# Performance work log

Measured on AMD Instinct MI355X. Metric: run time of the kernel, lower is better.

Reference implementation:

```python
import jax, jax.numpy as jnp
import numpy as np

DIM = 256
NUM_HEADS = 4
FRAMES = 8
B_ = 32768
INNER = DIM // 2              # 128
HEAD_DIM = INNER // NUM_HEADS # 32 (actual per-head dim in forward)
SCALE = (DIM // NUM_HEADS) ** -0.5  # faithful: init uses dim//num_heads = 64


def _rel_pos_index():
    # window_size = [FRAMES, 1, 1] -> index depends only on temporal offset
    d = np.arange(FRAMES)
    idx = d[:, None] - d[None, :] + (FRAMES - 1)  # [N, N] in [0, 2F-2]
    return jnp.asarray(idx, dtype=jnp.int32)


def setup_inputs() -> dict:
    key = jax.random.key(0)
    ks = jax.random.split(key, 5)
    x = jax.random.normal(ks[0], (B_, FRAMES, DIM), dtype=jnp.float32)
    qkv_w = jax.random.normal(ks[1], (DIM, INNER * 3), dtype=jnp.float32) * 0.02
    proj_w = jax.random.normal(ks[2], (INNER, DIM), dtype=jnp.float32) * 0.02
    proj_b = jnp.zeros((DIM,), dtype=jnp.float32)
    bias_table = jax.random.normal(ks[3], (2 * FRAMES - 1, NUM_HEADS), dtype=jnp.float32) * 0.02
    rel_index = _rel_pos_index()
    return {"x": x, "qkv_w": qkv_w, "proj_w": proj_w, "proj_b": proj_b,
            "bias_table": bias_table, "rel_index": rel_index}


def reference(x, qkv_w, proj_w, proj_b, bias_table, rel_index):
    B, N, C = x.shape
    h, hd = NUM_HEADS, HEAD_DIM
    qkv = (x @ qkv_w).reshape(B, N, 3, h, hd)
    qkv = jnp.transpose(qkv, (2, 0, 3, 1, 4))  # [3, B, h, N, hd]
    q, k, v = qkv[0], qkv[1], qkv[2]
    attn = jnp.einsum('bhnd,bhmd->bhnm', q * SCALE, k)  # [B, h, N, N]
    # gather relative position bias: [N, N, h] -> [h, N, N]
    bias = bias_table[rel_index[:N, :N]]  # [N, N, h]
    attn = attn + jnp.transpose(bias, (2, 0, 1))[None]
    attn = jax.nn.softmax(attn, axis=-1)
    out = jnp.einsum('bhnm,bhmd->bhnd', attn, v)       # [B, h, N, hd]
    out = jnp.transpose(out, (0, 2, 1, 3)).reshape(B, N, h * hd)  # [B, N, 128]
    return out @ proj_w + proj_b
```

## Files before the change

kernel.cpp:

```cpp
#include <hip/hip_runtime.h>
#include <hip/hip_bf16.h>

typedef short bf16x8 __attribute__((ext_vector_type(8)));
typedef float f32x4 __attribute__((ext_vector_type(4)));

#define B_TOT 32768
#define ROWS  128
#define NTHR  512

#define WSQ_ELT  0
#define WSP_ELT  98304

#define QK_STR   104
#define CH_STR   68
#define WQ_OFF   0
#define QK_OFF   24576
#define BIAS_OFF 59392
#define PB_OFF   60672
#define LDS_BYTES 61696

static __device__ __forceinline__ unsigned short f2b(float f) {
    __hip_bfloat16 h = __float2bfloat16(f);
    return reinterpret_cast<unsigned short&>(h);
}
static __device__ __forceinline__ float b2f(unsigned short u) {
    union { unsigned u; float f; } v; v.u = ((unsigned)u) << 16; return v.f;
}
static __device__ __forceinline__ void gload_lds16(const unsigned short* g, unsigned short* l) {
    __builtin_amdgcn_global_load_lds(
        (const __attribute__((address_space(1))) unsigned int*)g,
        (__attribute__((address_space(3))) unsigned int*)l, 16, 0, 0);
}

__global__ __launch_bounds__(256)
void prep_w(const float* __restrict__ qkv_w, const float* __restrict__ proj_w,
            unsigned short* __restrict__ ws)
{
    __shared__ float tile[64][65];
    const int bid = blockIdx.x;
    const float* src; unsigned short* dst; int ldw, ldk, tr0, tc0;
    if (bid < 24) {
        int kr = bid / 6, cg = bid % 6;
        src = qkv_w; dst = ws + WSQ_ELT; ldw = 384; ldk = 256;
        tr0 = kr * 64; tc0 = cg * 64;
    } else {
        int b = bid - 24; int kr = b / 4, cg = b % 4;
        src = proj_w; dst = ws + WSP_ELT; ldw = 256; ldk = 128;
        tr0 = kr * 64; tc0 = cg * 64;
    }
    const int t = threadIdx.x;
    #pragma unroll
    for (int i = 0; i < 16; ++i) {
        int idx = i * 256 + t;
        int r = idx >> 6, c = idx & 63;
        tile[r][c] = src[(size_t)(tr0 + r) * ldw + tc0 + c];
    }
    __syncthreads();
    #pragma unroll
    for (int i = 0; i < 2; ++i) {
        int idx = i * 256 + t;
        int c = idx >> 3, r0 = (idx & 7) * 8;
        union { unsigned short u[8]; uint4 v; } pk;
        #pragma unroll
        for (int j = 0; j < 8; ++j) pk.u[j] = f2b(tile[r0 + j][c]);
        *(uint4*)&dst[(size_t)(tc0 + c) * ldk + tr0 + r0] = pk.v;
    }
}

__global__ __launch_bounds__(NTHR, 4)
void ta_fused(const float* __restrict__ x,
              const unsigned short* __restrict__ ws,
              const float* __restrict__ proj_b,
              const float* __restrict__ bias_table,
              const int* __restrict__ rel_index,
              float* __restrict__ out)
{
    __shared__ __align__(16) char smem[LDS_BYTES];
    unsigned short* wqs = (unsigned short*)(smem + WQ_OFF);
    unsigned short* qks = (unsigned short*)(smem + QK_OFF);
    float* chunk  = (float*)(smem + QK_OFF);
    float* bias_s = (float*)(smem + BIAS_OFF);
    float* pbs    = (float*)(smem + PB_OFF);

    const unsigned short* wsq = ws + WSQ_ELT;
    const unsigned short* wsp = ws + WSP_ELT;

    const int tid = threadIdx.x;
    const int l   = tid & 63;
    const int w   = tid >> 6;
    const int l15 = l & 15;
    const int l4  = l >> 4;
    const long wg = blockIdx.x;

    bf16x8 af[8];
    {
        const float* xr = x + wg * (size_t)(ROWS * 256) + (size_t)(16 * w + l15) * 256;
        #pragma unroll
        for (int s = 0; s < 8; ++s) {
            f32x4 d0 = *(const f32x4*)(xr + s * 32 + l4 * 8);
            f32x4 d1 = *(const f32x4*)(xr + s * 32 + l4 * 8 + 4);
            union { unsigned short u[8]; bf16x8 v; } pk;
            #pragma unroll
            for (int j = 0; j < 4; ++j) pk.u[j] = f2b(d0[j]);
            #pragma unroll
            for (int j = 0; j < 4; ++j) pk.u[4 + j] = f2b(d1[j]);
            af[s] = pk.v;
        }
    }
    if (tid < 256) {
        int n = tid >> 5, m = (tid >> 2) & 7, hh = tid & 3;
        int ri = rel_index[n * 8 + m];
        bias_s[n * 40 + m * 5 + hh] = bias_table[ri * 4 + hh];
        pbs[tid] = proj_b[tid];
    }

    bf16x8 of0, of1, of2, of3;
    const f32x4 zero4 = {0.f, 0.f, 0.f, 0.f};

    #pragma unroll 1
    for (int h = 0; h < 4; ++h) {
        f32x4 acc[6];
        #pragma unroll
        for (int i = 0; i < 6; ++i) acc[i] = zero4;

        #pragma unroll
        for (int c = 0; c < 2; ++c) {
            __syncthreads();
            #pragma unroll
            for (int u = 0; u < 3; ++u) {
                int idx = u * NTHR + tid;
                int rr = idx >> 4, seg = idx & 15;
                int p = rr >> 5, wi = rr & 31;
                gload_lds16(&wsq[(size_t)(p * 128 + h * 32 + wi) * 256 + c * 128
                                 + ((seg ^ (rr & 7)) << 3)],
                            &wqs[rr * 128 + seg * 8]);
            }
            __syncthreads();
            #pragma unroll
            for (int ks2 = 0; ks2 < 4; ++ks2) {
                bf16x8 a = af[c * 4 + ks2];
                #pragma unroll
                for (int ct = 0; ct < 6; ++ct) {
                    int brow = ct * 16 + l15;
                    bf16x8 b = *(bf16x8*)&wqs[brow * 128 + (((ks2 * 4 + l4) ^ (brow & 7)) << 3)];
                    acc[ct] = __builtin_amdgcn_mfma_f32_16x16x32_bf16(a, b, acc[ct], 0, 0, 0);
                }
            }
        }
        #pragma unroll
        for (int ct = 0; ct < 6; ++ct)
          #pragma unroll
          for (int j = 0; j < 4; ++j) {
              int row = 16 * w + l4 * 4 + j;
              qks[row * QK_STR + ct * 16 + l15] = f2b(acc[ct][j]);
          }

        {
            const int r  = 16 * w + l15;
            const int rb = r & ~7;
            const int n  = r & 7;
            float qf[8];
            {
                bf16x8 qv = *(bf16x8*)&qks[r * QK_STR + l4 * 8];
                #pragma unroll
                for (int j = 0; j < 8; ++j) qf[j] = b2f((unsigned short)qv[j]);
            }
            float sp[8];
            #pragma unroll
            for (int m = 0; m < 8; ++m) {
                bf16x8 kv = *(bf16x8*)&qks[(rb + m) * QK_STR + 32 + l4 * 8];
                float s = 0.f;
                #pragma unroll
                for (int j = 0; j < 8; ++j) s += qf[j] * b2f((unsigned short)kv[j]);
                sp[m] = s;
            }
            #pragma unroll
            for (int m = 0; m < 8; ++m) {
                sp[m] += __shfl_xor(sp[m], 16);
                sp[m] += __shfl_xor(sp[m], 32);
            }
            float mx = -1e30f;
            #pragma unroll
            for (int m = 0; m < 8; ++m) {
                sp[m] = sp[m] * 0.125f + bias_s[n * 40 + m * 5 + h];
                mx = fmaxf(mx, sp[m]);
            }
            float sum = 0.f;
            #pragma unroll
            for (int m = 0; m < 8; ++m) { sp[m] = __expf(sp[m] - mx); sum += sp[m]; }
            float inv = 1.f / sum;
            float o[8] = {0.f,0.f,0.f,0.f,0.f,0.f,0.f,0.f};
            #pragma unroll
            for (int m = 0; m < 8; ++m) {
                bf16x8 vv = *(bf16x8*)&qks[(rb + m) * QK_STR + 64 + l4 * 8];
                #pragma unroll
                for (int j = 0; j < 8; ++j) o[j] += sp[m] * b2f((unsigned short)vv[j]);
            }
            bf16x8 ofr;
            #pragma unroll
            for (int j = 0; j < 8; ++j) ofr[j] = (short)f2b(o[j] * inv);
            if      (h == 0) of0 = ofr;
            else if (h == 1) of1 = ofr;
            else if (h == 2) of2 = ofr;
            else             of3 = ofr;
        }
    }

    __syncthreads();

    #pragma unroll 1
    for (int cc = 0; cc < 4; ++cc) {
        #pragma unroll
        for (int u = 0; u < 2; ++u) {
            int idx = u * NTHR + tid;
            int rr = idx >> 4, seg = idx & 15;
            gload_lds16(&wsp[(size_t)(cc * 64 + rr) * 128 + ((seg ^ (rr & 7)) << 3)],
                        &wqs[rr * 128 + seg * 8]);
        }
        __syncthreads();

        f32x4 acc2[4];
        #pragma unroll
        for (int i = 0; i < 4; ++i) acc2[i] = zero4;
        #pragma unroll
        for (int ctl = 0; ctl < 4; ++ctl) {
            int brow = ctl * 16 + l15;
            #pragma unroll
            for (int ks = 0; ks < 4; ++ks) {
                bf16x8 b = *(bf16x8*)&wqs[brow * 128 + (((ks * 4 + l4) ^ (brow & 7)) << 3)];
                bf16x8 a = (ks == 0) ? of0 : (ks == 1) ? of1 : (ks == 2) ? of2 : of3;
                acc2[ctl] = __builtin_amdgcn_mfma_f32_16x16x32_bf16(a, b, acc2[ctl], 0, 0, 0);
            }
        }
        #pragma unroll
        for (int ctl = 0; ctl < 4; ++ctl)
          #pragma unroll
          for (int j = 0; j < 4; ++j) {
              int row = 16 * w + l4 * 4 + j;
              int col = ctl * 16 + l15;
              chunk[row * CH_STR + col] = acc2[ctl][j] + pbs[cc * 64 + col];
          }
        __syncthreads();
        {
            float* og = out + wg * (size_t)(ROWS * 256) + cc * 64;
            #pragma unroll
            for (int i = 0; i < 4; ++i) {
                int f0 = i * NTHR + tid;
                int row = f0 >> 4, c4 = f0 & 15;
                f32x4 v = *(f32x4*)&chunk[row * CH_STR + c4 * 4];
                *(f32x4*)(og + (size_t)row * 256 + c4 * 4) = v;
            }
        }
    }
}

extern "C" void kernel_launch(void* const* d_in, const int* in_sizes, int n_in,
                              void* d_out, int out_size, void* d_ws, size_t ws_size,
                              hipStream_t stream)
{
    (void)in_sizes; (void)n_in; (void)ws_size; (void)out_size;
    const float* x  = (const float*)d_in[0];
    const float* qw = (const float*)d_in[1];
    const float* pw = (const float*)d_in[2];
    const float* pb = (const float*)d_in[3];
    const float* bt = (const float*)d_in[4];
    const int*   ri = (const int*)d_in[5];
    float* o = (float*)d_out;
    unsigned short* ws = (unsigned short*)d_ws;

    hipLaunchKernelGGL(prep_w, dim3(32), dim3(256), 0, stream, qw, pw, ws);
    hipLaunchKernelGGL(ta_fused, dim3(B_TOT / 16), dim3(NTHR), 0, stream,
                       x, ws, pb, bt, ri, o);
}
```

Baseline: 234.3 us.

## Double-buffer weight tiles in LDS to overlap global loads with MFMA

Splits the QKV and projection weight staging into half-width K chunks held in two LDS buffers. The next chunk is prefetched with global_load_lds while MFMAs consume the current one, and the prefetch chains across heads and into the projection phase. This aims to hide weight-load latency behind compute instead of stalling after each load. In exchange it adds more, smaller load phases and more complex barrier ordering.

```diff
diff --git a/kernel.cpp b/kernel.cpp
--- a/kernel.cpp
+++ b/kernel.cpp
@@ -11,10 +11,11 @@
 #define WSQ_ELT  0
 #define WSP_ELT  98304
 
+#define WQ0_OFF  0
+#define WQ1_OFF  12288
+#define QK_OFF   24576
 #define QK_STR   104
 #define CH_STR   68
-#define WQ_OFF   0
-#define QK_OFF   24576
 #define BIAS_OFF 59392
 #define PB_OFF   60672
 #define LDS_BYTES 61696
@@ -76,7 +77,8 @@
               float* __restrict__ out)
 {
     __shared__ __align__(16) char smem[LDS_BYTES];
-    unsigned short* wqs = (unsigned short*)(smem + WQ_OFF);
+    unsigned short* wq0 = (unsigned short*)(smem + WQ0_OFF);
+    unsigned short* wq1 = (unsigned short*)(smem + WQ1_OFF);
     unsigned short* qks = (unsigned short*)(smem + QK_OFF);
     float* chunk  = (float*)(smem + QK_OFF);
     float* bias_s = (float*)(smem + BIAS_OFF);
@@ -92,6 +94,32 @@
     const int l4  = l >> 4;
     const long wg = blockIdx.x;
 
+    auto stage1 = [&](int h, int c2, unsigned short* buf) {
+        {
+            int rr = tid >> 3, seg = tid & 7;
+            int p = rr >> 5, wi = rr & 31;
+            gload_lds16(&wsq[(size_t)(p * 128 + h * 32 + wi) * 256 + c2 * 64
+                             + ((seg ^ (rr & 7)) << 3)],
+                        &buf[rr * 64 + seg * 8]);
+        }
+        if (tid < 256) {
+            int idx = NTHR + tid;
+            int rr = idx >> 3, seg = idx & 7;
+            int p = rr >> 5, wi = rr & 31;
+            gload_lds16(&wsq[(size_t)(p * 128 + h * 32 + wi) * 256 + c2 * 64
+                             + ((seg ^ (rr & 7)) << 3)],
+                        &buf[rr * 64 + seg * 8]);
+        }
+    };
+    auto stage2 = [&](int cc, int kh, unsigned short* buf) {
+        int rr = tid >> 3, seg = tid & 7;
+        gload_lds16(&wsp[(size_t)(cc * 64 + rr) * 128 + kh * 64
+                         + ((seg ^ (rr & 7)) << 3)],
+                    &buf[rr * 64 + seg * 8]);
+    };
+
+    stage1(0, 0, wq0);
+
     bf16x8 af[8];
     {
         const float* xr = x + wg * (size_t)(ROWS * 256) + (size_t)(16 * w + l15) * 256;
@@ -124,25 +152,20 @@
         for (int i = 0; i < 6; ++i) acc[i] = zero4;
 
         #pragma unroll
-        for (int c = 0; c < 2; ++c) {
+        for (int c2 = 0; c2 < 4; ++c2) {
+            unsigned short* cur = (c2 & 1) ? wq1 : wq0;
+            unsigned short* nxt = (c2 & 1) ? wq0 : wq1;
             __syncthreads();
-            #pragma unroll
-            for (int u = 0; u < 3; ++u) {
-                int idx = u * NTHR + tid;
-                int rr = idx >> 4, seg = idx & 15;
-                int p = rr >> 5, wi = rr & 31;
-                gload_lds16(&wsq[(size_t)(p * 128 + h * 32 + wi) * 256 + c * 128
-                                 + ((seg ^ (rr & 7)) << 3)],
-                            &wqs[rr * 128 + seg * 8]);
-            }
-            __syncthreads();
-            #pragma unroll
-            for (int ks2 = 0; ks2 < 4; ++ks2) {
-                bf16x8 a = af[c * 4 + ks2];
+            if (c2 < 3)      stage1(h, c2 + 1, nxt);
+            else if (h < 3)  stage1(h + 1, 0, nxt);
+            else             stage2(0, 0, nxt);
+            #pragma unroll
+            for (int ks2 = 0; ks2 < 2; ++ks2) {
+                bf16x8 a = af[c2 * 2 + ks2];
                 #pragma unroll
                 for (int ct = 0; ct < 6; ++ct) {
                     int brow = ct * 16 + l15;
-                    bf16x8 b = *(bf16x8*)&wqs[brow * 128 + (((ks2 * 4 + l4) ^ (brow & 7)) << 3)];
+                    bf16x8 b = *(bf16x8*)&cur[brow * 64 + (((ks2 * 4 + l4) ^ (brow & 7)) << 3)];
                     acc[ct] = __builtin_amdgcn_mfma_f32_16x16x32_bf16(a, b, acc[ct], 0, 0, 0);
                 }
             }
@@ -206,29 +229,33 @@
         }
     }
 
-    __syncthreads();
-
     #pragma unroll 1
     for (int cc = 0; cc < 4; ++cc) {
-        #pragma unroll
-        for (int u = 0; u < 2; ++u) {
-            int idx = u * NTHR + tid;
-            int rr = idx >> 4, seg = idx & 15;
-            gload_lds16(&wsp[(size_t)(cc * 64 + rr) * 128 + ((seg ^ (rr & 7)) << 3)],
-                        &wqs[rr * 128 + seg * 8]);
-        }
         __syncthreads();
+        stage2(cc, 1, wq1);
 
         f32x4 acc2[4];
         #pragma unroll
         for (int i = 0; i < 4; ++i) acc2[i] = zero4;
         #pragma unroll
-        for (int ctl = 0; ctl < 4; ++ctl) {
-            int brow = ctl * 16 + l15;
-            #pragma unroll
-            for (int ks = 0; ks < 4; ++ks) {
-                bf16x8 b = *(bf16x8*)&wqs[brow * 128 + (((ks * 4 + l4) ^ (brow & 7)) << 3)];
-                bf16x8 a = (ks == 0) ? of0 : (ks == 1) ? of1 : (ks == 2) ? of2 : of3;
+        for (int ks = 0; ks < 2; ++ks) {
+            bf16x8 a = (ks == 0) ? of0 : of1;
+            #pragma unroll
+            for (int ctl = 0; ctl < 4; ++ctl) {
+                int brow = ctl * 16 + l15;
+                bf16x8 b = *(bf16x8*)&wq0[brow * 64 + (((ks * 4 + l4) ^ (brow & 7)) << 3)];
+                acc2[ctl] = __builtin_amdgcn_mfma_f32_16x16x32_bf16(a, b, acc2[ctl], 0, 0, 0);
+            }
+        }
+        __syncthreads();
+        if (cc < 3) stage2(cc + 1, 0, wq0);
+        #pragma unroll
+        for (int ks = 0; ks < 2; ++ks) {
+            bf16x8 a = (ks == 0) ? of2 : of3;
+            #pragma unroll
+            for (int ctl = 0; ctl < 4; ++ctl) {
+                int brow = ctl * 16 + l15;
+                bf16x8 b = *(bf16x8*)&wq1[brow * 64 + (((ks * 4 + l4) ^ (brow & 7)) << 3)];
                 acc2[ctl] = __builtin_amdgcn_mfma_f32_16x16x32_bf16(a, b, acc2[ctl], 0, 0, 0);
             }
         }
```

After: 214.6 us. -8.4%, faster.

## Double-buffer QKV and projection weight tiles in LDS to overlap loads

Applied to the files above, without the earlier changes.

Stages each head's full QKV weight slice (both K halves at once) and each projection chunk into alternating LDS buffers, prefetching the next stage while the MFMAs run on the current one. This removes a barrier and an exposed load per step. LDS use roughly doubles to about 127 KB, so the launch bound drops to 2 blocks per CU and occupancy falls, which may offset the latency hiding. Dynamic shared memory with a raised attribute is used instead of a static array.

```diff
diff --git a/kernel.cpp b/kernel.cpp
--- a/kernel.cpp
+++ b/kernel.cpp
@@ -11,13 +11,17 @@
 #define WSQ_ELT  0
 #define WSP_ELT  98304
 
+#define WQ_A     0
+#define WQ_B     49152
+#define G2_B0    0
+#define G2_B1    16384
+#define CH_OFF   49152
+#define CH_STR   68
+#define QK_OFF   98304
 #define QK_STR   104
-#define CH_STR   68
-#define WQ_OFF   0
-#define QK_OFF   24576
-#define BIAS_OFF 59392
-#define PB_OFF   60672
-#define LDS_BYTES 61696
+#define BIAS_OFF 124928
+#define PB_OFF   126208
+#define LDS_BYTES 127232
 
 static __device__ __forceinline__ unsigned short f2b(float f) {
     __hip_bfloat16 h = __float2bfloat16(f);
@@ -67,7 +71,7 @@
     }
 }
 
-__global__ __launch_bounds__(NTHR, 4)
+__global__ __launch_bounds__(NTHR, 2)
 void ta_fused(const float* __restrict__ x,
               const unsigned short* __restrict__ ws,
               const float* __restrict__ proj_b,
@@ -75,10 +79,13 @@
               const int* __restrict__ rel_index,
               float* __restrict__ out)
 {
-    __shared__ __align__(16) char smem[LDS_BYTES];
-    unsigned short* wqs = (unsigned short*)(smem + WQ_OFF);
+    extern __shared__ __align__(16) char smem[];
+    unsigned short* wqA = (unsigned short*)(smem + WQ_A);
+    unsigned short* wqB = (unsigned short*)(smem + WQ_B);
+    unsigned short* g2b0 = (unsigned short*)(smem + G2_B0);
+    unsigned short* g2b1 = (unsigned short*)(smem + G2_B1);
     unsigned short* qks = (unsigned short*)(smem + QK_OFF);
-    float* chunk  = (float*)(smem + QK_OFF);
+    float* chunk  = (float*)(smem + CH_OFF);
     float* bias_s = (float*)(smem + BIAS_OFF);
     float* pbs    = (float*)(smem + PB_OFF);
 
@@ -92,6 +99,30 @@
     const int l4  = l >> 4;
     const long wg = blockIdx.x;
 
+    auto stage1 = [&](int h, unsigned short* buf) {
+        #pragma unroll
+        for (int u = 0; u < 6; ++u) {
+            int idx = u * NTHR + tid;
+            int rr = idx >> 5, slot = idx & 31;
+            int c  = slot ^ (rr & 7);
+            int p  = rr >> 5, wi = rr & 31;
+            gload_lds16(&wsq[(size_t)(p * 128 + h * 32 + wi) * 256 + c * 8],
+                        &buf[rr * 256 + slot * 8]);
+        }
+    };
+    auto stage2 = [&](int cc, unsigned short* buf) {
+        #pragma unroll
+        for (int u = 0; u < 2; ++u) {
+            int idx = u * NTHR + tid;
+            int rr = idx >> 4, slot = idx & 15;
+            int c  = slot ^ (rr & 7);
+            gload_lds16(&wsp[(size_t)(cc * 64 + rr) * 128 + c * 8],
+                        &buf[rr * 128 + slot * 8]);
+        }
+    };
+
+    stage1(0, wqA);
+
     bf16x8 af[8];
     {
         const float* xr = x + wg * (size_t)(ROWS * 256) + (size_t)(16 * w + l15) * 256;
@@ -119,30 +150,24 @@
 
     #pragma unroll 1
     for (int h = 0; h < 4; ++h) {
+        unsigned short* cur = (h & 1) ? wqB : wqA;
+        __syncthreads();
+        if (h < 3) stage1(h + 1, (h & 1) ? wqA : wqB);
+        else       stage2(0, g2b0);
+
         f32x4 acc[6];
         #pragma unroll
         for (int i = 0; i < 6; ++i) acc[i] = zero4;
-
-        #pragma unroll
-        for (int c = 0; c < 2; ++c) {
-            __syncthreads();
-            #pragma unroll
-            for (int u = 0; u < 3; ++u) {
-                int idx = u * NTHR + tid;
-                int rr = idx >> 4, seg = idx & 15;
-                int p = rr >> 5, wi = rr & 31;
-                gload_lds16(&wsq[(size_t)(p * 128 + h * 32 + wi) * 256 + c * 128
-                                 + ((seg ^ (rr & 7)) << 3)],
-                            &wqs[rr * 128 + seg * 8]);
-            }
-            __syncthreads();
-            #pragma unroll
-            for (int ks2 = 0; ks2 < 4; ++ks2) {
-                bf16x8 a = af[c * 4 + ks2];
+        #pragma unroll
+        for (int c2 = 0; c2 < 4; ++c2) {
+            #pragma unroll
+            for (int ks2 = 0; ks2 < 2; ++ks2) {
+                bf16x8 a = af[c2 * 2 + ks2];
                 #pragma unroll
                 for (int ct = 0; ct < 6; ++ct) {
                     int brow = ct * 16 + l15;
-                    bf16x8 b = *(bf16x8*)&wqs[brow * 128 + (((ks2 * 4 + l4) ^ (brow & 7)) << 3)];
+                    int g = c2 * 8 + ks2 * 4 + l4;
+                    bf16x8 b = *(bf16x8*)&cur[brow * 256 + ((g ^ (brow & 7)) << 3)];
                     acc[ct] = __builtin_amdgcn_mfma_f32_16x16x32_bf16(a, b, acc[ct], 0, 0, 0);
                 }
             }
@@ -206,18 +231,11 @@
         }
     }
 
-    __syncthreads();
-
     #pragma unroll 1
     for (int cc = 0; cc < 4; ++cc) {
-        #pragma unroll
-        for (int u = 0; u < 2; ++u) {
-            int idx = u * NTHR + tid;
-            int rr = idx >> 4, seg = idx & 15;
-            gload_lds16(&wsp[(size_t)(cc * 64 + rr) * 128 + ((seg ^ (rr & 7)) << 3)],
-                        &wqs[rr * 128 + seg * 8]);
-        }
+        unsigned short* cur = (cc & 1) ? g2b1 : g2b0;
         __syncthreads();
+        if (cc < 3) stage2(cc + 1, (cc & 1) ? g2b0 : g2b1);
 
         f32x4 acc2[4];
         #pragma unroll
@@ -227,7 +245,8 @@
             int brow = ctl * 16 + l15;
             #pragma unroll
             for (int ks = 0; ks < 4; ++ks) {
-                bf16x8 b = *(bf16x8*)&wqs[brow * 128 + (((ks * 4 + l4) ^ (brow & 7)) << 3)];
+                int g = ks * 4 + l4;
+                bf16x8 b = *(bf16x8*)&cur[brow * 128 + ((g ^ (brow & 7)) << 3)];
                 bf16x8 a = (ks == 0) ? of0 : (ks == 1) ? of1 : (ks == 2) ? of2 : of3;
                 acc2[ctl] = __builtin_amdgcn_mfma_f32_16x16x32_bf16(a, b, acc2[ctl], 0, 0, 0);
             }
@@ -268,7 +287,10 @@
     float* o = (float*)d_out;
     unsigned short* ws = (unsigned short*)d_ws;
 
+    (void)hipFuncSetAttribute((const void*)ta_fused,
+                              hipFuncAttributeMaxDynamicSharedMemorySize, LDS_BYTES);
+
     hipLaunchKernelGGL(prep_w, dim3(32), dim3(256), 0, stream, qw, pw, ws);
-    hipLaunchKernelGGL(ta_fused, dim3(B_TOT / 16), dim3(NTHR), 0, stream,
+    hipLaunchKernelGGL(ta_fused, dim3(B_TOT / 16), dim3(NTHR), LDS_BYTES, stream,
                        x, ws, pb, bt, ri, o);
 }
```

Result: slower. 244.3 us (+4.3%).
